# Optimization experiments

Measured on AMD Instinct MI355X. Metric: run time of the kernel, lower is better.

## Reference

```python
import jax, jax.numpy as jnp
import numpy as np

M, IN, H, OUT = 64, 3, 256, 3
B = 8192
W0_FIRST = 30.0
W0_HIDDEN = 30.0


def setup_inputs() -> dict:
    key = jax.random.key(0)
    ks = jax.random.split(key, 12)
    fb = 1.0 / IN                                   # first-layer bound
    hb = np.sqrt(6.0 / H) / W0_HIDDEN               # hidden bound
    x = jax.random.uniform(ks[0], (B, IN), jnp.float32, -1.0, 1.0)
    w0 = jax.random.uniform(ks[1], (M, H, IN), jnp.float32, -fb, fb)
    b0 = jnp.zeros((M, H), jnp.float32)
    w1 = jax.random.uniform(ks[2], (M, H, H), jnp.float32, -hb, hb)
    b1 = jnp.zeros((M, H), jnp.float32)
    w2 = jax.random.uniform(ks[3], (M, H, H), jnp.float32, -hb, hb)
    b2 = jnp.zeros((M, H), jnp.float32)
    w3 = jax.random.uniform(ks[4], (M, H, H), jnp.float32, -hb, hb)
    b3 = jnp.zeros((M, H), jnp.float32)
    wf = jax.random.uniform(ks[5], (M, OUT, H), jnp.float32, -hb, hb)
    bf = jnp.zeros((M, OUT), jnp.float32)
    return {"x": x, "w0": w0, "b0": b0, "w1": w1, "b1": b1,
            "w2": w2, "b2": b2, "w3": w3, "b3": b3, "wf": wf, "bf": bf}


def reference(x, w0, b0, w1, b1, w2, b2, w3, b3, wf, bf):
    # first sine layer: [B,in] x [M,H,in] -> [B,M,H]
    h = jnp.sin(W0_FIRST * (jnp.einsum('bi,moi->bmo', x, w0) + b0[None]))
    # hidden sine layers
    for w, b in ((w1, b1), (w2, b2), (w3, b3)):
        h = jnp.sin(W0_HIDDEN * (jnp.einsum('bmi,moi->bmo', h, w) + b[None]))
    # final linear: [B,M,H] x [M,out,H] -> [B,M,out]
    return jnp.einsum('bmi,moi->bmo', h, wf) + bf[None]
```

## Files before the change

kernel.cpp:

```cpp
#include <hip/hip_runtime.h>

#define MEXP  64
#define HDIM  256
#define INDIM 3
#define ODIM  3
#define BT    64
#define NTILE 128
#define SINSC 4.774648292756860f

typedef __attribute__((ext_vector_type(8))) _Float16 f16x8;
typedef __attribute__((ext_vector_type(4))) _Float16 f16x4;
typedef __attribute__((ext_vector_type(4))) float    f32x4;

__device__ __forceinline__ int swz(int row, int byteInRow) {
  return (row * 512 + byteInRow) ^ (((row ^ (row >> 3)) & 7) << 4);
}

__global__ void prep_hidden(const float* __restrict__ w1, const float* __restrict__ w2,
                            const float* __restrict__ w3, _Float16* __restrict__ ws) {
  int chunk = blockIdx.x * 256 + threadIdx.x;
  int lm    = chunk >> 13;
  int c     = chunk & 8191;
  int layer = lm >> 6, m = lm & 63;
  int lane  = c & 63;
  int ctks  = c >> 6;
  int ct = ctks >> 3, ks = ctks & 7;
  int col = ct * 16 + (lane & 15);
  int k   = ks * 32 + ((lane >> 4) << 3);
  const float* w = (layer == 0) ? w1 : (layer == 1) ? w2 : w3;
  const float* src = w + ((size_t)m * HDIM + col) * HDIM + k;
  f16x8 v;
#pragma unroll
  for (int j = 0; j < 8; ++j) v[j] = (_Float16)(src[j] * SINSC);
  *(f16x8*)(ws + (size_t)chunk * 8) = v;
}

__global__ void prep_wf(const float* __restrict__ wf, _Float16* __restrict__ ws) {
  int chunk = blockIdx.x * 256 + threadIdx.x;
  int m    = chunk >> 9;
  int c    = chunk & 511;
  int lane = c & 63;
  int ks   = c >> 6;
  int col  = lane & 15;
  int k    = ks * 32 + ((lane >> 4) << 3);
  f16x8 v;
  if (col < ODIM) {
    const float* src = wf + ((size_t)m * ODIM + col) * HDIM + k;
#pragma unroll
    for (int j = 0; j < 8; ++j) v[j] = (_Float16)src[j];
  } else {
#pragma unroll
    for (int j = 0; j < 8; ++j) v[j] = (_Float16)0.0f;
  }
  *(f16x8*)(ws + (size_t)chunk * 8) = v;
}

__device__ __forceinline__ void hidden_layer(char* hb, const _Float16* __restrict__ wl,
                                             const float* __restrict__ bptr,
                                             int wid, int lane, int g) {
  f32x4 acc[4][4];
#pragma unroll
  for (int ct = 0; ct < 4; ++ct) {
    f32x4 binit = *(const f32x4*)(bptr + wid * 64 + ct * 16 + g * 4);
    binit *= SINSC;
#pragma unroll
    for (int rt = 0; rt < 4; ++rt) acc[rt][ct] = binit;
  }
  const f16x8* wfrag = (const f16x8*)wl;
  f16x8 A[4];
#pragma unroll
  for (int ct = 0; ct < 4; ++ct)
    A[ct] = wfrag[((wid * 4 + ct) * 8 + 0) * 64 + lane];
#pragma unroll
  for (int ks = 0; ks < 8; ++ks) {
    f16x8 a[4];
#pragma unroll
    for (int ct = 0; ct < 4; ++ct) a[ct] = A[ct];
    if (ks < 7) {
#pragma unroll
      for (int ct = 0; ct < 4; ++ct)
        A[ct] = wfrag[((wid * 4 + ct) * 8 + ks + 1) * 64 + lane];
    }
#pragma unroll
    for (int rt = 0; rt < 4; ++rt) {
      f16x8 b = *(const f16x8*)(hb + swz(rt * 16 + (lane & 15), ks * 64 + g * 16));
#pragma unroll
      for (int ct = 0; ct < 4; ++ct)
        acc[rt][ct] = __builtin_amdgcn_mfma_f32_16x16x32_f16(a[ct], b, acc[rt][ct], 0, 0, 0);
    }
  }
  __syncthreads();
#pragma unroll
  for (int ct = 0; ct < 4; ++ct) {
    int c0 = wid * 64 + ct * 16 + g * 4;
#pragma unroll
    for (int rt = 0; rt < 4; ++rt) {
      f16x4 v;
#pragma unroll
      for (int t = 0; t < 4; ++t)
        v[t] = (_Float16)__builtin_amdgcn_sinf(acc[rt][ct][t]);
      *(f16x4*)(hb + swz(rt * 16 + (lane & 15), c0 * 2)) = v;
    }
  }
  __syncthreads();
}

__global__ __launch_bounds__(256, 2)
void siren_fused(const float* __restrict__ x, const float* __restrict__ w0,
                 const float* __restrict__ b0, const float* __restrict__ b1,
                 const float* __restrict__ b2, const float* __restrict__ b3,
                 const float* __restrict__ bfin, const _Float16* __restrict__ wh,
                 const _Float16* __restrict__ wff, float* __restrict__ out) {
  __shared__ _Float16 hbuf[BT * HDIM];
  char* hb = (char*)hbuf;

  int tid  = threadIdx.x;
  int lane = tid & 63;
  int wid  = tid >> 6;
  int g    = lane >> 4;
  int id   = blockIdx.x;
  int m    = ((id & 7) << 3) + ((id >> 3) >> 7);
  int tile = (id >> 3) & (NTILE - 1);

  {
    int col = tid;
    const float* wp = w0 + ((size_t)m * HDIM + col) * INDIM;
    float wc0 = wp[0], wc1 = wp[1], wc2 = wp[2];
    float bc  = b0[m * HDIM + col] * SINSC;
    const float* xp = x + (size_t)tile * BT * INDIM;
#pragma unroll 4
    for (int r = 0; r < BT; ++r) {
      float z = fmaf(xp[r * 3 + 2], wc2, fmaf(xp[r * 3 + 1], wc1, xp[r * 3] * wc0));
      float h = __builtin_amdgcn_sinf(fmaf(z, SINSC, bc));
      *(_Float16*)(hb + swz(r, col * 2)) = (_Float16)h;
    }
  }
  __syncthreads();

  hidden_layer(hb, wh + ((size_t)0 * MEXP + m) * (HDIM * HDIM), b1 + m * HDIM, wid, lane, g);
  hidden_layer(hb, wh + ((size_t)1 * MEXP + m) * (HDIM * HDIM), b2 + m * HDIM, wid, lane, g);
  hidden_layer(hb, wh + ((size_t)2 * MEXP + m) * (HDIM * HDIM), b3 + m * HDIM, wid, lane, g);

  {
    f32x4 facc = {};
    const f16x8* wfrag = (const f16x8*)(wff + (size_t)m * (16 * HDIM));
#pragma unroll
    for (int ks = 0; ks < 8; ++ks) {
      f16x8 b = *(const f16x8*)(hb + swz(wid * 16 + (lane & 15), ks * 64 + g * 16));
      f16x8 a = wfrag[ks * 64 + lane];
      facc = __builtin_amdgcn_mfma_f32_16x16x32_f16(a, b, facc, 0, 0, 0);
    }
    if (g == 0) {
      size_t r = (size_t)tile * BT + wid * 16 + (lane & 15);
#pragma unroll
      for (int t = 0; t < 3; ++t)
        out[(r * MEXP + m) * ODIM + t] = facc[t] + bfin[m * ODIM + t];
    }
  }
}

extern "C" void kernel_launch(void* const* d_in, const int* in_sizes, int n_in,
                              void* d_out, int out_size, void* d_ws, size_t ws_size,
                              hipStream_t stream) {
  (void)in_sizes; (void)n_in; (void)out_size; (void)ws_size;
  const float* x  = (const float*)d_in[0];
  const float* w0 = (const float*)d_in[1];
  const float* b0 = (const float*)d_in[2];
  const float* w1 = (const float*)d_in[3];
  const float* b1 = (const float*)d_in[4];
  const float* w2 = (const float*)d_in[5];
  const float* b2 = (const float*)d_in[6];
  const float* w3 = (const float*)d_in[7];
  const float* b3 = (const float*)d_in[8];
  const float* wf = (const float*)d_in[9];
  const float* bf = (const float*)d_in[10];

  _Float16* wh  = (_Float16*)d_ws;
  _Float16* wff = wh + (size_t)3 * MEXP * HDIM * HDIM;

  prep_hidden<<<6144, 256, 0, stream>>>(w1, w2, w3, wh);
  prep_wf<<<128, 256, 0, stream>>>(wf, wff);
  siren_fused<<<8192, 256, 0, stream>>>(x, w0, b0, b1, b2, b3, bf, wh, wff, (float*)d_out);
}
```

Baseline: 375.7 us.

## Compute first SIREN layer with MFMA using split-fp16 operands and prefetch next-layer weights

```diff
diff --git a/kernel.cpp b/kernel.cpp
--- a/kernel.cpp
+++ b/kernel.cpp
@@ -55,7 +55,48 @@
   *(f16x8*)(ws + (size_t)chunk * 8) = v;
 }
 
-__device__ __forceinline__ void hidden_layer(char* hb, const _Float16* __restrict__ wl,
+__global__ void prep_w0(const float* __restrict__ w0, _Float16* __restrict__ ws) {
+  int c    = blockIdx.x * 256 + threadIdx.x;
+  int m    = c >> 10;
+  int ct   = (c >> 6) & 15;
+  int lane = c & 63;
+  int col  = ct * 16 + (lane & 15);
+  int g    = lane >> 4;
+  const float* src = w0 + ((size_t)m * HDIM + col) * INDIM;
+  f16x8 v = {};
+  if (g == 0 || g == 2) {
+#pragma unroll
+    for (int j = 0; j < 3; ++j) v[j] = (_Float16)(src[j] * SINSC);
+  } else if (g == 1) {
+#pragma unroll
+    for (int j = 0; j < 3; ++j) {
+      float w = src[j] * SINSC;
+      _Float16 hi = (_Float16)w;
+      v[j] = (_Float16)(w - (float)hi);
+    }
+  }
+  *(f16x8*)(ws + (size_t)c * 8) = v;
+}
+
+__device__ __forceinline__ void epilogue_sin(char* hb, f32x4 (&acc)[4][4],
+                                             int wid, int lane, int g) {
+#pragma unroll
+  for (int ct = 0; ct < 4; ++ct) {
+    int c0 = wid * 64 + ct * 16 + g * 4;
+#pragma unroll
+    for (int rt = 0; rt < 4; ++rt) {
+      f16x4 v;
+#pragma unroll
+      for (int t = 0; t < 4; ++t)
+        v[t] = (_Float16)__builtin_amdgcn_sinf(acc[rt][ct][t]);
+      *(f16x4*)(hb + swz(rt * 16 + (lane & 15), c0 * 2)) = v;
+    }
+  }
+}
+
+__device__ __forceinline__ void hidden_layer(char* hb, f16x8 (&A)[4],
+                                             const _Float16* __restrict__ wl,
+                                             const f16x8* __restrict__ nextp, int ns,
                                              const float* __restrict__ bptr,
                                              int wid, int lane, int g) {
   f32x4 acc[4][4];
@@ -67,10 +108,6 @@
     for (int rt = 0; rt < 4; ++rt) acc[rt][ct] = binit;
   }
   const f16x8* wfrag = (const f16x8*)wl;
-  f16x8 A[4];
-#pragma unroll
-  for (int ct = 0; ct < 4; ++ct)
-    A[ct] = wfrag[((wid * 4 + ct) * 8 + 0) * 64 + lane];
 #pragma unroll
   for (int ks = 0; ks < 8; ++ks) {
     f16x8 a[4];
@@ -89,29 +126,21 @@
         acc[rt][ct] = __builtin_amdgcn_mfma_f32_16x16x32_f16(a[ct], b, acc[rt][ct], 0, 0, 0);
     }
   }
+#pragma unroll
+  for (int ct = 0; ct < 4; ++ct) A[ct] = nextp[ct * ns];
   __syncthreads();
-#pragma unroll
-  for (int ct = 0; ct < 4; ++ct) {
-    int c0 = wid * 64 + ct * 16 + g * 4;
-#pragma unroll
-    for (int rt = 0; rt < 4; ++rt) {
-      f16x4 v;
-#pragma unroll
-      for (int t = 0; t < 4; ++t)
-        v[t] = (_Float16)__builtin_amdgcn_sinf(acc[rt][ct][t]);
-      *(f16x4*)(hb + swz(rt * 16 + (lane & 15), c0 * 2)) = v;
-    }
-  }
+  epilogue_sin(hb, acc, wid, lane, g);
   __syncthreads();
 }
 
 __global__ __launch_bounds__(256, 2)
-void siren_fused(const float* __restrict__ x, const float* __restrict__ w0,
-                 const float* __restrict__ b0, const float* __restrict__ b1,
-                 const float* __restrict__ b2, const float* __restrict__ b3,
-                 const float* __restrict__ bfin, const _Float16* __restrict__ wh,
+void siren_fused(const float* __restrict__ x, const float* __restrict__ b0,
+                 const float* __restrict__ b1, const float* __restrict__ b2,
+                 const float* __restrict__ b3, const float* __restrict__ bfin,
+                 const _Float16* __restrict__ w0f, const _Float16* __restrict__ wh,
                  const _Float16* __restrict__ wff, float* __restrict__ out) {
-  __shared__ _Float16 hbuf[BT * HDIM];
+  __shared__ __align__(16) _Float16 hbuf[BT * HDIM];
+  __shared__ __align__(16) _Float16 xbuf[BT * 40];
   char* hb = (char*)hbuf;
 
   int tid  = threadIdx.x;
@@ -122,33 +151,79 @@
   int m    = ((id & 7) << 3) + ((id >> 3) >> 7);
   int tile = (id >> 3) & (NTILE - 1);
 
+  const f16x8* w0p = (const f16x8*)(w0f + (size_t)m * (16 * 64 * 8));
+  f16x8 A[4];
+#pragma unroll
+  for (int ct = 0; ct < 4; ++ct) A[ct] = w0p[(wid * 4 + ct) * 64 + lane];
+
   {
-    int col = tid;
-    const float* wp = w0 + ((size_t)m * HDIM + col) * INDIM;
-    float wc0 = wp[0], wc1 = wp[1], wc2 = wp[2];
-    float bc  = b0[m * HDIM + col] * SINSC;
-    const float* xp = x + (size_t)tile * BT * INDIM;
-#pragma unroll 4
-    for (int r = 0; r < BT; ++r) {
-      float z = fmaf(xp[r * 3 + 2], wc2, fmaf(xp[r * 3 + 1], wc1, xp[r * 3] * wc0));
-      float h = __builtin_amdgcn_sinf(fmaf(z, SINSC, bc));
-      *(_Float16*)(hb + swz(r, col * 2)) = (_Float16)h;
-    }
+    int row = tid & 63, which = tid >> 6;
+    const float* xp = x + ((size_t)tile * BT + row) * INDIM;
+    f16x8 v = {};
+    if (which < 2) {
+#pragma unroll
+      for (int j = 0; j < 3; ++j) v[j] = (_Float16)xp[j];
+    } else if (which == 2) {
+#pragma unroll
+      for (int j = 0; j < 3; ++j) {
+        float xv = xp[j];
+        _Float16 hi = (_Float16)xv;
+        v[j] = (_Float16)(xv - (float)hi);
+      }
+    }
+    *(f16x8*)((char*)xbuf + row * 80 + which * 16) = v;
   }
   __syncthreads();
 
-  hidden_layer(hb, wh + ((size_t)0 * MEXP + m) * (HDIM * HDIM), b1 + m * HDIM, wid, lane, g);
-  hidden_layer(hb, wh + ((size_t)1 * MEXP + m) * (HDIM * HDIM), b2 + m * HDIM, wid, lane, g);
-  hidden_layer(hb, wh + ((size_t)2 * MEXP + m) * (HDIM * HDIM), b3 + m * HDIM, wid, lane, g);
+  const _Float16* wl1 = wh + ((size_t)0 * MEXP + m) * (HDIM * HDIM);
+  const _Float16* wl2 = wh + ((size_t)1 * MEXP + m) * (HDIM * HDIM);
+  const _Float16* wl3 = wh + ((size_t)2 * MEXP + m) * (HDIM * HDIM);
+  const f16x8*    wfp = (const f16x8*)(wff + (size_t)m * (16 * HDIM));
 
   {
+    f32x4 acc[4][4];
+#pragma unroll
+    for (int ct = 0; ct < 4; ++ct) {
+      f32x4 binit = *(const f32x4*)(b0 + m * HDIM + wid * 64 + ct * 16 + g * 4);
+      binit *= SINSC;
+#pragma unroll
+      for (int rt = 0; rt < 4; ++rt) acc[rt][ct] = binit;
+    }
+#pragma unroll
+    for (int rt = 0; rt < 4; ++rt) {
+      f16x8 b = *(const f16x8*)((char*)xbuf + (rt * 16 + (lane & 15)) * 80 + g * 16);
+#pragma unroll
+      for (int ct = 0; ct < 4; ++ct)
+        acc[rt][ct] = __builtin_amdgcn_mfma_f32_16x16x32_f16(A[ct], b, acc[rt][ct], 0, 0, 0);
+    }
+    const f16x8* np = (const f16x8*)wl1 + wid * 2048 + lane;
+#pragma unroll
+    for (int ct = 0; ct < 4; ++ct) A[ct] = np[ct * 512];
+    epilogue_sin(hb, acc, wid, lane, g);
+    __syncthreads();
+  }
+
+  hidden_layer(hb, A, wl1, (const f16x8*)wl2 + wid * 2048 + lane, 512,
+               b1 + m * HDIM, wid, lane, g);
+  hidden_layer(hb, A, wl2, (const f16x8*)wl3 + wid * 2048 + lane, 512,
+               b2 + m * HDIM, wid, lane, g);
+  hidden_layer(hb, A, wl3, wfp + lane, 64,
+               b3 + m * HDIM, wid, lane, g);
+
+  {
+    f16x8 A2[4];
+#pragma unroll
+    for (int ct = 0; ct < 4; ++ct) A2[ct] = wfp[(4 + ct) * 64 + lane];
     f32x4 facc = {};
-    const f16x8* wfrag = (const f16x8*)(wff + (size_t)m * (16 * HDIM));
-#pragma unroll
-    for (int ks = 0; ks < 8; ++ks) {
+#pragma unroll
+    for (int ks = 0; ks < 4; ++ks) {
       f16x8 b = *(const f16x8*)(hb + swz(wid * 16 + (lane & 15), ks * 64 + g * 16));
-      f16x8 a = wfrag[ks * 64 + lane];
-      facc = __builtin_amdgcn_mfma_f32_16x16x32_f16(a, b, facc, 0, 0, 0);
+      facc = __builtin_amdgcn_mfma_f32_16x16x32_f16(A[ks], b, facc, 0, 0, 0);
+    }
+#pragma unroll
+    for (int ks = 4; ks < 8; ++ks) {
+      f16x8 b = *(const f16x8*)(hb + swz(wid * 16 + (lane & 15), ks * 64 + g * 16));
+      facc = __builtin_amdgcn_mfma_f32_16x16x32_f16(A2[ks - 4], b, facc, 0, 0, 0);
     }
     if (g == 0) {
       size_t r = (size_t)tile * BT + wid * 16 + (lane & 15);
@@ -177,8 +252,11 @@
 
   _Float16* wh  = (_Float16*)d_ws;
   _Float16* wff = wh + (size_t)3 * MEXP * HDIM * HDIM;
+  _Float16* w0f = wff + (size_t)MEXP * 16 * HDIM;
 
   prep_hidden<<<6144, 256, 0, stream>>>(w1, w2, w3, wh);
   prep_wf<<<128, 256, 0, stream>>>(wf, wff);
-  siren_fused<<<8192, 256, 0, stream>>>(x, w0, b0, b1, b2, b3, bf, wh, wff, (float*)d_out);
-}
+  prep_w0<<<256, 256, 0, stream>>>(w0, w0f);
+  siren_fused<<<8192, 256, 0, stream>>>(x, b0, b1, b2, b3, bf, w0f, wh, wff,
+                                        (float*)d_out);
+}
```

After: 335.6 us. 1.12x faster.
